# Optimization experiments

Measured on AMD Instinct MI355X. Metric: run time of the kernel, lower is better.

## Reference

```python
import jax, jax.numpy as jnp
import numpy as np
from math import sqrt

B, Q, S, D, H = 2, 2048, 2048, 1024, 16
ADIM = D // H
IEPS = 1e-32


def setup_inputs() -> dict:
    key = jax.random.key(0)
    ks = jax.random.split(key, 7)
    sc = 0.02
    return {
        "iQ": jax.random.normal(ks[0], (B, Q, D), jnp.float32),
        "iK": jax.random.normal(ks[1], (B, S, D), jnp.float32),
        "mask": jax.random.randint(ks[2], (B, Q, S), 0, 2) > 0,
        "Wq": jax.random.normal(ks[3], (D, D), jnp.float32) * sc,
        "Wkv": jax.random.normal(ks[4], (2 * D, D), jnp.float32) * sc,
        "Wo": jax.random.normal(ks[5], (D, D), jnp.float32) * sc,
        "nbias": jnp.zeros((1,), jnp.float32),
    }


def sparse_norm(scores, nbias):
    # ReLU(x + b)^2 normalized along last axis (SparseNormer)
    t = jax.nn.relu(scores + nbias[0])
    t = t * t
    return t / (t.sum(-1, keepdims=True) + IEPS)


def reference(iQ, iK, mask, Wq, Wkv, Wo, nbias):
    b, q, _ = iQ.shape
    s = iK.shape[1]
    # projections (no bias)
    rq = (iQ @ Wq.T).reshape(b, q, H, ADIM)            # bqhd
    kv = (iK @ Wkv.T).reshape(b, s, 2, H, ADIM)
    rk, rv = kv[:, :, 0], kv[:, :, 1]                  # bshd each
    scores = jnp.einsum("bqhd,bshd->bhqs", rq, rk) / sqrt(ADIM)
    scores = jnp.where(mask[:, None, :, :], jnp.float32(-1e32), scores)
    attn = sparse_norm(scores, nbias)
    o = jnp.einsum("bhqs,bshd->bqhd", attn, rv).reshape(b, q, H * ADIM)
    return o @ Wo.T
```

## Files before the change

### kernel.cpp

```cpp
#include <hip/hip_runtime.h>

#define Bb 2
#define Qq 2048
#define Ss 2048
#define Dd 1024
#define Hh 16
#define AD 64
#define KK 1024

typedef __attribute__((ext_vector_type(8))) short bf16x8;
typedef __attribute__((ext_vector_type(4))) short bf16x4;
typedef __attribute__((ext_vector_type(4))) float f32x4;
typedef unsigned short u16;
typedef unsigned int u32;
typedef unsigned long long u64;

__device__ __forceinline__ u16 f2bf(float f) {
  union { float f; u32 u; } v; v.f = f;
  u32 r = v.u + 0x7fffu + ((v.u >> 16) & 1u);
  return (u16)(r >> 16);
}

__device__ __forceinline__ void gld16(const u16* g, u16* l) {
  __builtin_amdgcn_global_load_lds(
      (const __attribute__((address_space(1))) unsigned int*)g,
      (__attribute__((address_space(3))) unsigned int*)l, 16, 0, 0);
}

__global__ __launch_bounds__(256) void cast_all_k(const float* __restrict__ iQ,
                                                  const float* __restrict__ iK,
                                                  const float* __restrict__ Wq,
                                                  const float* __restrict__ Wkv,
                                                  const float* __restrict__ Wo,
                                                  u16* __restrict__ Qb, u16* __restrict__ Kb,
                                                  u16* __restrict__ Wqb, u16* __restrict__ Wkvb,
                                                  u16* __restrict__ Wob) {
  int i = blockIdx.x * 256 + threadIdx.x;
  const float* src; u16* dst; int off;
  if (i < 1048576)      { src = iQ;  dst = Qb;   off = 0; }
  else if (i < 2097152) { src = iK;  dst = Kb;   off = 1048576; }
  else if (i < 2359296) { src = Wq;  dst = Wqb;  off = 2097152; }
  else if (i < 2883584) { src = Wkv; dst = Wkvb; off = 2359296; }
  else                  { src = Wo;  dst = Wob;  off = 2883584; }
  int j = i - off;
  float4 v = ((const float4*)src)[j];
  ushort4 o;
  o.x = f2bf(v.x); o.y = f2bf(v.y); o.z = f2bf(v.z); o.w = f2bf(v.w);
  ((ushort4*)dst)[j] = o;
}

__global__ __launch_bounds__(256) void maskpack_k(const int* __restrict__ mask,
                                                  u64* __restrict__ mb64) {
  int flat = blockIdx.x * 256 + threadIdx.x;
  int st = flat & 31;
  int q  = (flat >> 5) & 2047;
  int b  = flat >> 16;
  const int4* src = (const int4*)(mask + ((size_t)(b * Qq + q)) * Ss + st * 64);
  u64 bits = 0;
#pragma unroll
  for (int c = 0; c < 16; c++) {
    int4 v = src[c];
    bits |= (u64)(v.x != 0) << (c * 4 + 0);
    bits |= (u64)(v.y != 0) << (c * 4 + 1);
    bits |= (u64)(v.z != 0) << (c * 4 + 2);
    bits |= (u64)(v.w != 0) << (c * 4 + 3);
  }
  mb64[flat] = bits;
}

__global__ __launch_bounds__(256, 4) void proj_k(const u16* __restrict__ Qb,
                                                 const u16* __restrict__ Kb,
                                                 const u16* __restrict__ Wqb,
                                                 const u16* __restrict__ Wkvb,
                                                 u16* __restrict__ RQ,
                                                 u16* __restrict__ KV,
                                                 u16* __restrict__ VT) {
  __shared__ u16 LDS[128 * 64 + 64 * 64];
  u16* As = LDS;
  u16* Ws = LDS + 128 * 64;
  u16* Tt = LDS;
  const int tid = threadIdx.x;
  const int lane = tid & 63, wave = tid >> 6;
  const int qr = lane & 15, quad = lane >> 4;
  const int bid = blockIdx.x;
  const bool isQ = bid < 512;
  const int b2 = isQ ? bid : bid - 512;
  const int m0 = (b2 & 31) * 128;
  const int n0 = (b2 >> 5) * 64;
  const u16* A = isQ ? Qb : Kb;
  const u16* W = isQ ? Wqb : Wkvb;
  const int wm = (wave >> 1) * 64, wn = (wave & 1) * 32;
  const int qs = qr & 7;

  const int sr = tid >> 3, sc = tid & 7;
  const u16 *aP[4], *wP[2];
  u16 *aL[4], *wL[2];
#pragma unroll
  for (int is = 0; is < 4; is++) {
    int row = is * 32 + sr;
    aP[is] = A + (size_t)(m0 + row) * KK + ((sc ^ (row & 7)) * 8);
    aL[is] = As + row * 64 + sc * 8;
  }
#pragma unroll
  for (int is = 0; is < 2; is++) {
    int row = is * 32 + sr;
    wP[is] = W + (size_t)(n0 + row) * KK + ((sc ^ (row & 7)) * 8);
    wL[is] = Ws + row * 64 + sc * 8;
  }

  f32x4 acc[4][2] = {};

  for (int k0 = 0; k0 < KK; k0 += 64) {
#pragma unroll
    for (int is = 0; is < 4; is++) gld16(aP[is] + k0, aL[is]);
#pragma unroll
    for (int is = 0; is < 2; is++) gld16(wP[is] + k0, wL[is]);
    __syncthreads();
#pragma unroll
    for (int kk = 0; kk < 2; kk++) {
      bf16x8 af[4], bw[2];
#pragma unroll
      for (int i = 0; i < 4; i++)
        af[i] = *(const bf16x8*)(As + (wm + i * 16 + qr) * 64 + (((kk * 4 + quad) ^ qs) * 8));
#pragma unroll
      for (int j = 0; j < 2; j++)
        bw[j] = *(const bf16x8*)(Ws + (wn + j * 16 + qr) * 64 + (((kk * 4 + quad) ^ qs) * 8));
#pragma unroll
      for (int i = 0; i < 4; i++)
#pragma unroll
        for (int j = 0; j < 2; j++)
          acc[i][j] = __builtin_amdgcn_mfma_f32_16x16x32_bf16(af[i], bw[j], acc[i][j], 0, 0, 0);
    }
    __syncthreads();
  }

  if (isQ) {
#pragma unroll
    for (int i = 0; i < 4; i++)
#pragma unroll
      for (int j = 0; j < 2; j++)
#pragma unroll
        for (int r = 0; r < 4; r++) {
          int row = m0 + wm + i * 16 + quad * 4 + r;
          int col = n0 + wn + j * 16 + qr;
          RQ[(size_t)row * 1024 + col] = f2bf(acc[i][j][r] * 0.125f);
        }
  } else if (n0 < 1024) {
#pragma unroll
    for (int i = 0; i < 4; i++)
#pragma unroll
      for (int j = 0; j < 2; j++)
#pragma unroll
        for (int r = 0; r < 4; r++) {
          int row = m0 + wm + i * 16 + quad * 4 + r;
          int col = n0 + wn + j * 16 + qr;
          KV[(size_t)row * 2048 + col] = f2bf(acc[i][j][r]);
        }
  } else {
#pragma unroll
    for (int i = 0; i < 4; i++)
#pragma unroll
      for (int j = 0; j < 2; j++)
#pragma unroll
        for (int r = 0; r < 4; r++) {
          int srow = wm + i * 16 + quad * 4 + r;
          int d    = wn + j * 16 + qr;
          Tt[d * 136 + srow] = f2bf(acc[i][j][r]);
        }
    __syncthreads();
    const int h = (n0 - 1024) >> 6;
    const int bb = m0 >> 11, sbase = m0 & 2047;
    u16* vdst = VT + (((size_t)(bb * Hh + h)) * AD) * Ss;
    const int d = tid >> 2;
#pragma unroll
    for (int ic = 0; ic < 4; ic++) {
      int ch = ic * 4 + (tid & 3);
      *(int4*)(vdst + (size_t)d * Ss + sbase + ch * 8) = *(const int4*)(Tt + d * 136 + ch * 8);
    }
  }
}

__global__ __launch_bounds__(256, 4) void oproj_k(const u16* __restrict__ A,
                                                  const u16* __restrict__ W,
                                                  float* __restrict__ C) {
  __shared__ u16 LDS[128 * 64 + 64 * 64];
  u16* As = LDS;
  u16* Ws = LDS + 128 * 64;
  const int tid = threadIdx.x;
  const int lane = tid & 63, wave = tid >> 6;
  const int qr = lane & 15, quad = lane >> 4;
  const int m0 = (blockIdx.x & 31) * 128;
  const int n0 = (blockIdx.x >> 5) * 64;
  const int wm = (wave >> 1) * 64, wn = (wave & 1) * 32;
  const int qs = qr & 7;
  const int sr = tid >> 3, sc = tid & 7;
  const u16 *aP[4], *wP[2];
  u16 *aL[4], *wL[2];
#pragma unroll
  for (int is = 0; is < 4; is++) {
    int row = is * 32 + sr;
    aP[is] = A + (size_t)(m0 + row) * KK + ((sc ^ (row & 7)) * 8);
    aL[is] = As + row * 64 + sc * 8;
  }
#pragma unroll
  for (int is = 0; is < 2; is++) {
    int row = is * 32 + sr;
    wP[is] = W + (size_t)(n0 + row) * KK + ((sc ^ (row & 7)) * 8);
    wL[is] = Ws + row * 64 + sc * 8;
  }
  f32x4 acc[4][2] = {};
  for (int k0 = 0; k0 < KK; k0 += 64) {
#pragma unroll
    for (int is = 0; is < 4; is++) gld16(aP[is] + k0, aL[is]);
#pragma unroll
    for (int is = 0; is < 2; is++) gld16(wP[is] + k0, wL[is]);
    __syncthreads();
#pragma unroll
    for (int kk = 0; kk < 2; kk++) {
      bf16x8 af[4], bw[2];
#pragma unroll
      for (int i = 0; i < 4; i++)
        af[i] = *(const bf16x8*)(As + (wm + i * 16 + qr) * 64 + (((kk * 4 + quad) ^ qs) * 8));
#pragma unroll
      for (int j = 0; j < 2; j++)
        bw[j] = *(const bf16x8*)(Ws + (wn + j * 16 + qr) * 64 + (((kk * 4 + quad) ^ qs) * 8));
#pragma unroll
      for (int i = 0; i < 4; i++)
#pragma unroll
        for (int j = 0; j < 2; j++)
          acc[i][j] = __builtin_amdgcn_mfma_f32_16x16x32_bf16(af[i], bw[j], acc[i][j], 0, 0, 0);
    }
    __syncthreads();
  }
#pragma unroll
  for (int i = 0; i < 4; i++)
#pragma unroll
    for (int j = 0; j < 2; j++)
#pragma unroll
      for (int r = 0; r < 4; r++) {
        int row = m0 + wm + i * 16 + quad * 4 + r;
        int col = n0 + wn + j * 16 + qr;
        C[(size_t)row * 1024 + col] = acc[i][j][r];
      }
}

__global__ __launch_bounds__(512, 4) void attn_k(const u16* __restrict__ RQ,
                                                 const u16* __restrict__ KV,
                                                 const u16* __restrict__ VT,
                                                 const u64* __restrict__ mb64,
                                                 const float* __restrict__ nbias,
                                                 u16* __restrict__ O) {
  __shared__ char LB[65536];
  u16* Ks  = (u16*)LB;
  u16* Vts = (u16*)(LB + 32768);
  f32x4* Xch = (f32x4*)LB;

  const int tid = threadIdx.x, lane = tid & 63, w = tid >> 6;
  const int qh = w >> 1, sh = w & 1;
  const int qr = lane & 15, quad = lane >> 4;
  const int quad4 = quad * 4, qs = qr & 7;
  const int q0 = blockIdx.x * 128, h = blockIdx.y, b = blockIdx.z;
  const u16* rqb = RQ + ((size_t)(b * Qq + q0)) * Dd + h * AD;
  const u16* kb  = KV + ((size_t)b * Ss) * 2048 + h * AD;
  const u16* vtb = VT + ((size_t)(b * Hh + h)) * AD * Ss;
  const u64* mbase = mb64 + ((size_t)(b * Qq + q0)) * 32;
  const float nb = nbias[0];

  bf16x8 bq[2][2];
#pragma unroll
  for (int j = 0; j < 2; j++)
#pragma unroll
    for (int kk = 0; kk < 2; kk++)
      bq[j][kk] = *(const bf16x8*)(rqb + (size_t)(qh * 32 + j * 16 + qr) * Dd +
                                   kk * 32 + quad * 8);

  const u16 *kP[4], *vP[4];
  u16 *kL[4], *vL[4];
  {
    const int r8 = tid >> 3, c8 = tid & 7;
#pragma unroll
    for (int is = 0; is < 4; is++) {
      int row = is * 64 + r8;
      kP[is] = kb + (size_t)row * 2048 + ((c8 ^ (row & 7)) * 8);
      kL[is] = Ks + row * 64 + c8 * 8;
    }
    const int r32 = tid >> 5, c32 = tid & 31;
#pragma unroll
    for (int is = 0; is < 4; is++) {
      int row = is * 16 + r32;
      vP[is] = vtb + (size_t)row * Ss + ((c32 ^ (row & 7)) * 8);
      vL[is] = Vts + row * 256 + c32 * 8;
    }
  }

  const bf16x4 vones = { (short)0x3F80, (short)0x3F80, (short)0x3F80, (short)0x3F80 };
  f32x4 acc[2][4] = {};
  f32x4 accd[2] = {};

  const u16* kfr = Ks + (sh * 128 + qr) * 64;
  const u16* kfr0 = kfr + ((quad ^ qs) * 8);
  const u16* kfr1 = kfr + (((quad + 4) ^ qs) * 8);

  for (int t = 0; t < 8; t++) {
    __syncthreads();
#pragma unroll
    for (int is = 0; is < 4; is++) gld16(kP[is] + (size_t)t * 524288, kL[is]);
#pragma unroll
    for (int is = 0; is < 4; is++) gld16(vP[is] + t * 256, vL[is]);
    u64 mw[2][2];
#pragma unroll
    for (int j = 0; j < 2; j++) {
      const u64* mp = mbase + (size_t)(qh * 32 + j * 16 + qr) * 32 + t * 4 + sh * 2;
      mw[j][0] = mp[0];
      mw[j][1] = mp[1];
    }
    __syncthreads();

#pragma unroll
    for (int mi = 0; mi < 8; mi++) {
      bf16x8 ak0 = *(const bf16x8*)(kfr0 + mi * 1024);
      bf16x8 ak1 = *(const bf16x8*)(kfr1 + mi * 1024);
      f32x4 asc0 = { nb, nb, nb, nb };
      f32x4 asc1 = { nb, nb, nb, nb };
      asc0 = __builtin_amdgcn_mfma_f32_16x16x32_bf16(ak0, bq[0][0], asc0, 0, 0, 0);
      asc0 = __builtin_amdgcn_mfma_f32_16x16x32_bf16(ak1, bq[0][1], asc0, 0, 0, 0);
      asc1 = __builtin_amdgcn_mfma_f32_16x16x32_bf16(ak0, bq[1][0], asc1, 0, 0, 0);
      asc1 = __builtin_amdgcn_mfma_f32_16x16x32_bf16(ak1, bq[1][1], asc1, 0, 0, 0);

      union { u32 w2[2]; bf16x4 v; } pk[2];
#pragma unroll
      for (int j = 0; j < 2; j++) {
        f32x4 asc = j ? asc1 : asc0;
        u32 mm = (u32)(mw[j][mi >> 2] >> ((mi & 3) * 16 + quad4)) & 0xFu;
        u32 th[4];
#pragma unroll
        for (int r = 0; r < 4; r++) {
          float tt = fmaxf(asc[r], 0.f);
          tt = tt * tt;
          if ((mm >> r) & 1) tt = 0.f;
          union { float f; u32 u; } cv; cv.f = tt;
          th[r] = cv.u;
        }
        pk[j].w2[0] = __builtin_amdgcn_perm(th[1], th[0], 0x07060302u);
        pk[j].w2[1] = __builtin_amdgcn_perm(th[3], th[2], 0x07060302u);
        accd[j] = __builtin_amdgcn_mfma_f32_16x16x16bf16_1k(pk[j].v, vones, accd[j], 0, 0, 0);
      }
      int g = ((sh * 32 + mi * 4 + quad) ^ (qs << 1)) * 4;
#pragma unroll
      for (int nn = 0; nn < 4; nn++) {
        bf16x4 bv = *(const bf16x4*)(Vts + (nn * 16 + qr) * 256 + g);
        acc[0][nn] = __builtin_amdgcn_mfma_f32_16x16x16bf16_1k(pk[0].v, bv, acc[0][nn], 0, 0, 0);
        acc[1][nn] = __builtin_amdgcn_mfma_f32_16x16x16bf16_1k(pk[1].v, bv, acc[1][nn], 0, 0, 0);
      }
    }
  }

  __syncthreads();
  if (sh == 1) {
#pragma unroll
    for (int j = 0; j < 2; j++) {
#pragma unroll
      for (int nn = 0; nn < 4; nn++)
        Xch[qh * 640 + (j * 4 + nn) * 64 + lane] = acc[j][nn];
      Xch[qh * 640 + (8 + j) * 64 + lane] = accd[j];
    }
  }
  __syncthreads();
  if (sh == 0) {
    u16* ob = O + ((size_t)(b * Qq + q0)) * Dd + h * AD;
#pragma unroll
    for (int j = 0; j < 2; j++) {
      f32x4 dpart = Xch[qh * 640 + (8 + j) * 64 + lane];
      float rc[4];
#pragma unroll
      for (int r = 0; r < 4; r++)
        rc[r] = 1.f / (accd[j][r] + dpart[r] + 1e-32f);
#pragma unroll
      for (int nn = 0; nn < 4; nn++) {
        f32x4 p4 = Xch[qh * 640 + (j * 4 + nn) * 64 + lane];
#pragma unroll
        for (int r = 0; r < 4; r++) {
          int ql = qh * 32 + j * 16 + quad * 4 + r;
          ob[(size_t)ql * Dd + nn * 16 + qr] = f2bf((acc[j][nn][r] + p4[r]) * rc[r]);
        }
      }
    }
  }
}

extern "C" void kernel_launch(void* const* d_in, const int* in_sizes, int n_in,
                              void* d_out, int out_size, void* d_ws, size_t ws_size,
                              hipStream_t stream) {
  const float* iQ   = (const float*)d_in[0];
  const float* iK   = (const float*)d_in[1];
  const int*   mask = (const int*)d_in[2];
  const float* Wq   = (const float*)d_in[3];
  const float* Wkv  = (const float*)d_in[4];
  const float* Wo   = (const float*)d_in[5];
  const float* nb   = (const float*)d_in[6];

  char* ws = (char*)d_ws;
  u16* Qb   = (u16*)(ws + (size_t)0);
  u16* Kb   = (u16*)(ws + ((size_t)8  << 20));
  u16* Wqb  = (u16*)(ws + ((size_t)16 << 20));
  u16* Wkvb = (u16*)(ws + ((size_t)18 << 20));
  u16* Wob  = (u16*)(ws + ((size_t)22 << 20));
  u16* RQ   = (u16*)(ws + ((size_t)24 << 20));
  u16* KV   = (u16*)(ws + ((size_t)32 << 20));
  u16* Obuf = (u16*)(ws + ((size_t)48 << 20));
  u16* VT   = (u16*)(ws + ((size_t)56 << 20));
  u64* MB   = (u64*)(ws + ((size_t)64 << 20));

  cast_all_k<<<12288, 256, 0, stream>>>(iQ, iK, Wq, Wkv, Wo, Qb, Kb, Wqb, Wkvb, Wob);
  maskpack_k<<<512, 256, 0, stream>>>(mask, MB);

  proj_k<<<1536, 256, 0, stream>>>(Qb, Kb, Wqb, Wkvb, RQ, KV, VT);

  attn_k<<<dim3(16, 16, 2), 512, 0, stream>>>(RQ, KV, VT, MB, nb, Obuf);

  oproj_k<<<512, 256, 0, stream>>>(Obuf, Wob, (float*)d_out);
}
```

Before: 229.3 us.

## Enlarge GEMM tiles to 128x128, compact K buffer, merge mask pack into cast

Projection and output GEMMs move from 128x64 to 128x128 block tiles, so each wave computes 64x64 and the number of blocks halves. This raises MFMA work per LDS load and cuts redundant global reads of the A operand, at the cost of more accumulator registers, which is why the occupancy hint drops from 4 to 3. The K projection is now written to a compact 1024-wide buffer instead of a 2048-stride KV buffer, so attention reads K with a tighter stride. The mask-packing kernel is folded into the cast kernel to save one launch.

```diff
diff --git a/kernel.cpp b/kernel.cpp
--- a/kernel.cpp
+++ b/kernel.cpp
@@ -32,103 +32,101 @@
                                                   const float* __restrict__ Wq,
                                                   const float* __restrict__ Wkv,
                                                   const float* __restrict__ Wo,
+                                                  const int* __restrict__ mask,
                                                   u16* __restrict__ Qb, u16* __restrict__ Kb,
                                                   u16* __restrict__ Wqb, u16* __restrict__ Wkvb,
-                                                  u16* __restrict__ Wob) {
+                                                  u16* __restrict__ Wob,
+                                                  u64* __restrict__ mb64) {
   int i = blockIdx.x * 256 + threadIdx.x;
-  const float* src; u16* dst; int off;
-  if (i < 1048576)      { src = iQ;  dst = Qb;   off = 0; }
-  else if (i < 2097152) { src = iK;  dst = Kb;   off = 1048576; }
-  else if (i < 2359296) { src = Wq;  dst = Wqb;  off = 2097152; }
-  else if (i < 2883584) { src = Wkv; dst = Wkvb; off = 2359296; }
-  else                  { src = Wo;  dst = Wob;  off = 2883584; }
-  int j = i - off;
-  float4 v = ((const float4*)src)[j];
-  ushort4 o;
-  o.x = f2bf(v.x); o.y = f2bf(v.y); o.z = f2bf(v.z); o.w = f2bf(v.w);
-  ((ushort4*)dst)[j] = o;
-}
-
-__global__ __launch_bounds__(256) void maskpack_k(const int* __restrict__ mask,
-                                                  u64* __restrict__ mb64) {
-  int flat = blockIdx.x * 256 + threadIdx.x;
-  int st = flat & 31;
-  int q  = (flat >> 5) & 2047;
-  int b  = flat >> 16;
-  const int4* src = (const int4*)(mask + ((size_t)(b * Qq + q)) * Ss + st * 64);
-  u64 bits = 0;
-#pragma unroll
-  for (int c = 0; c < 16; c++) {
-    int4 v = src[c];
-    bits |= (u64)(v.x != 0) << (c * 4 + 0);
-    bits |= (u64)(v.y != 0) << (c * 4 + 1);
-    bits |= (u64)(v.z != 0) << (c * 4 + 2);
-    bits |= (u64)(v.w != 0) << (c * 4 + 3);
-  }
-  mb64[flat] = bits;
-}
-
-__global__ __launch_bounds__(256, 4) void proj_k(const u16* __restrict__ Qb,
+  if (i < 3145728) {
+    const float* src; u16* dst; int off;
+    if (i < 1048576)      { src = iQ;  dst = Qb;   off = 0; }
+    else if (i < 2097152) { src = iK;  dst = Kb;   off = 1048576; }
+    else if (i < 2359296) { src = Wq;  dst = Wqb;  off = 2097152; }
+    else if (i < 2883584) { src = Wkv; dst = Wkvb; off = 2359296; }
+    else                  { src = Wo;  dst = Wob;  off = 2883584; }
+    int j = i - off;
+    float4 v = ((const float4*)src)[j];
+    ushort4 o;
+    o.x = f2bf(v.x); o.y = f2bf(v.y); o.z = f2bf(v.z); o.w = f2bf(v.w);
+    ((ushort4*)dst)[j] = o;
+  } else {
+    int flat = i - 3145728;
+    int st = flat & 31;
+    int q  = (flat >> 5) & 2047;
+    int b  = flat >> 16;
+    const int4* src = (const int4*)(mask + ((size_t)(b * Qq + q)) * Ss + st * 64);
+    u64 bits = 0;
+#pragma unroll
+    for (int c = 0; c < 16; c++) {
+      int4 v = src[c];
+      bits |= (u64)(v.x != 0) << (c * 4 + 0);
+      bits |= (u64)(v.y != 0) << (c * 4 + 1);
+      bits |= (u64)(v.z != 0) << (c * 4 + 2);
+      bits |= (u64)(v.w != 0) << (c * 4 + 3);
+    }
+    mb64[flat] = bits;
+  }
+}
+
+__global__ __launch_bounds__(256, 3) void proj_k(const u16* __restrict__ Qb,
                                                  const u16* __restrict__ Kb,
                                                  const u16* __restrict__ Wqb,
                                                  const u16* __restrict__ Wkvb,
                                                  u16* __restrict__ RQ,
-                                                 u16* __restrict__ KV,
+                                                 u16* __restrict__ Kc,
                                                  u16* __restrict__ VT) {
-  __shared__ u16 LDS[128 * 64 + 64 * 64];
-  u16* As = LDS;
-  u16* Ws = LDS + 128 * 64;
-  u16* Tt = LDS;
+  __shared__ char LB[34816];
+  u16* As = (u16*)LB;
+  u16* Ws = (u16*)(LB + 16384);
   const int tid = threadIdx.x;
   const int lane = tid & 63, wave = tid >> 6;
   const int qr = lane & 15, quad = lane >> 4;
+  const int qs = qr & 7;
   const int bid = blockIdx.x;
-  const bool isQ = bid < 512;
-  const int b2 = isQ ? bid : bid - 512;
+  const bool isQ = bid < 256;
+  const int b2 = isQ ? bid : bid - 256;
   const int m0 = (b2 & 31) * 128;
-  const int n0 = (b2 >> 5) * 64;
+  const int n0 = (b2 >> 5) * 128;
   const u16* A = isQ ? Qb : Kb;
   const u16* W = isQ ? Wqb : Wkvb;
-  const int wm = (wave >> 1) * 64, wn = (wave & 1) * 32;
-  const int qs = qr & 7;
+  const int wm = (wave >> 1) * 64, wn = (wave & 1) * 64;
 
   const int sr = tid >> 3, sc = tid & 7;
-  const u16 *aP[4], *wP[2];
-  u16 *aL[4], *wL[2];
+  const u16 *aP[4], *wP[4];
+  u16 *aL[4], *wL[4];
 #pragma unroll
   for (int is = 0; is < 4; is++) {
     int row = is * 32 + sr;
-    aP[is] = A + (size_t)(m0 + row) * KK + ((sc ^ (row & 7)) * 8);
+    int goff = (sc ^ (row & 7)) * 8;
+    aP[is] = A + (size_t)(m0 + row) * KK + goff;
+    wP[is] = W + (size_t)(n0 + row) * KK + goff;
     aL[is] = As + row * 64 + sc * 8;
-  }
-#pragma unroll
-  for (int is = 0; is < 2; is++) {
-    int row = is * 32 + sr;
-    wP[is] = W + (size_t)(n0 + row) * KK + ((sc ^ (row & 7)) * 8);
     wL[is] = Ws + row * 64 + sc * 8;
   }
 
-  f32x4 acc[4][2] = {};
+  f32x4 acc[4][4] = {};
 
   for (int k0 = 0; k0 < KK; k0 += 64) {
 #pragma unroll
     for (int is = 0; is < 4; is++) gld16(aP[is] + k0, aL[is]);
 #pragma unroll
-    for (int is = 0; is < 2; is++) gld16(wP[is] + k0, wL[is]);
+    for (int is = 0; is < 4; is++) gld16(wP[is] + k0, wL[is]);
     __syncthreads();
 #pragma unroll
     for (int kk = 0; kk < 2; kk++) {
-      bf16x8 af[4], bw[2];
+      bf16x8 af[4], bw[4];
+      int ch = ((kk * 4 + quad) ^ qs) * 8;
 #pragma unroll
       for (int i = 0; i < 4; i++)
-        af[i] = *(const bf16x8*)(As + (wm + i * 16 + qr) * 64 + (((kk * 4 + quad) ^ qs) * 8));
-#pragma unroll
-      for (int j = 0; j < 2; j++)
-        bw[j] = *(const bf16x8*)(Ws + (wn + j * 16 + qr) * 64 + (((kk * 4 + quad) ^ qs) * 8));
+        af[i] = *(const bf16x8*)(As + (wm + i * 16 + qr) * 64 + ch);
+#pragma unroll
+      for (int j = 0; j < 4; j++)
+        bw[j] = *(const bf16x8*)(Ws + (wn + j * 16 + qr) * 64 + ch);
 #pragma unroll
       for (int i = 0; i < 4; i++)
 #pragma unroll
-        for (int j = 0; j < 2; j++)
+        for (int j = 0; j < 4; j++)
           acc[i][j] = __builtin_amdgcn_mfma_f32_16x16x32_bf16(af[i], bw[j], acc[i][j], 0, 0, 0);
     }
     __syncthreads();
@@ -138,7 +136,7 @@
 #pragma unroll
     for (int i = 0; i < 4; i++)
 #pragma unroll
-      for (int j = 0; j < 2; j++)
+      for (int j = 0; j < 4; j++)
 #pragma unroll
         for (int r = 0; r < 4; r++) {
           int row = m0 + wm + i * 16 + quad * 4 + r;
@@ -149,85 +147,84 @@
 #pragma unroll
     for (int i = 0; i < 4; i++)
 #pragma unroll
-      for (int j = 0; j < 2; j++)
+      for (int j = 0; j < 4; j++)
 #pragma unroll
         for (int r = 0; r < 4; r++) {
           int row = m0 + wm + i * 16 + quad * 4 + r;
           int col = n0 + wn + j * 16 + qr;
-          KV[(size_t)row * 2048 + col] = f2bf(acc[i][j][r]);
+          Kc[(size_t)row * 1024 + col] = f2bf(acc[i][j][r]);
         }
   } else {
+    u16* Ttp = (u16*)LB + (wn >> 6) * (64 * 136);
 #pragma unroll
     for (int i = 0; i < 4; i++)
 #pragma unroll
-      for (int j = 0; j < 2; j++)
+      for (int j = 0; j < 4; j++)
 #pragma unroll
         for (int r = 0; r < 4; r++) {
           int srow = wm + i * 16 + quad * 4 + r;
-          int d    = wn + j * 16 + qr;
-          Tt[d * 136 + srow] = f2bf(acc[i][j][r]);
+          int d    = j * 16 + qr;
+          Ttp[d * 136 + srow] = f2bf(acc[i][j][r]);
         }
     __syncthreads();
-    const int h = (n0 - 1024) >> 6;
+    const int h0 = (n0 - 1024) >> 6;
     const int bb = m0 >> 11, sbase = m0 & 2047;
-    u16* vdst = VT + (((size_t)(bb * Hh + h)) * AD) * Ss;
-    const int d = tid >> 2;
-#pragma unroll
-    for (int ic = 0; ic < 4; ic++) {
-      int ch = ic * 4 + (tid & 3);
-      *(int4*)(vdst + (size_t)d * Ss + sbase + ch * 8) = *(const int4*)(Tt + d * 136 + ch * 8);
-    }
-  }
-}
-
-__global__ __launch_bounds__(256, 4) void oproj_k(const u16* __restrict__ A,
+    const u16* LB16 = (const u16*)LB;
+#pragma unroll
+    for (int ic = 0; ic < 8; ic++) {
+      int flat = ic * 256 + tid;
+      int hd = flat >> 10, d = (flat >> 4) & 63, ch = flat & 15;
+      *(int4*)(VT + (((size_t)(bb * Hh + h0 + hd)) * AD + d) * Ss + sbase + ch * 8) =
+          *(const int4*)(LB16 + hd * (64 * 136) + d * 136 + ch * 8);
+    }
+  }
+}
+
+__global__ __launch_bounds__(256, 3) void oproj_k(const u16* __restrict__ A,
                                                   const u16* __restrict__ W,
                                                   float* __restrict__ C) {
-  __shared__ u16 LDS[128 * 64 + 64 * 64];
-  u16* As = LDS;
-  u16* Ws = LDS + 128 * 64;
+  __shared__ u16 As[128 * 64];
+  __shared__ u16 Ws[128 * 64];
   const int tid = threadIdx.x;
   const int lane = tid & 63, wave = tid >> 6;
   const int qr = lane & 15, quad = lane >> 4;
+  const int qs = qr & 7;
   const int m0 = (blockIdx.x & 31) * 128;
-  const int n0 = (blockIdx.x >> 5) * 64;
-  const int wm = (wave >> 1) * 64, wn = (wave & 1) * 32;
-  const int qs = qr & 7;
+  const int n0 = (blockIdx.x >> 5) * 128;
+  const int wm = (wave >> 1) * 64, wn = (wave & 1) * 64;
   const int sr = tid >> 3, sc = tid & 7;
-  const u16 *aP[4], *wP[2];
-  u16 *aL[4], *wL[2];
+  const u16 *aP[4], *wP[4];
+  u16 *aL[4], *wL[4];
 #pragma unroll
   for (int is = 0; is < 4; is++) {
     int row = is * 32 + sr;
-    aP[is] = A + (size_t)(m0 + row) * KK + ((sc ^ (row & 7)) * 8);
+    int goff = (sc ^ (row & 7)) * 8;
+    aP[is] = A + (size_t)(m0 + row) * KK + goff;
+    wP[is] = W + (size_t)(n0 + row) * KK + goff;
     aL[is] = As + row * 64 + sc * 8;
-  }
-#pragma unroll
-  for (int is = 0; is < 2; is++) {
-    int row = is * 32 + sr;
-    wP[is] = W + (size_t)(n0 + row) * KK + ((sc ^ (row & 7)) * 8);
     wL[is] = Ws + row * 64 + sc * 8;
   }
-  f32x4 acc[4][2] = {};
+  f32x4 acc[4][4] = {};
   for (int k0 = 0; k0 < KK; k0 += 64) {
 #pragma unroll
     for (int is = 0; is < 4; is++) gld16(aP[is] + k0, aL[is]);
 #pragma unroll
-    for (int is = 0; is < 2; is++) gld16(wP[is] + k0, wL[is]);
+    for (int is = 0; is < 4; is++) gld16(wP[is] + k0, wL[is]);
     __syncthreads();
 #pragma unroll
     for (int kk = 0; kk < 2; kk++) {
-      bf16x8 af[4], bw[2];
+      bf16x8 af[4], bw[4];
+      int ch = ((kk * 4 + quad) ^ qs) * 8;
 #pragma unroll
       for (int i = 0; i < 4; i++)
-        af[i] = *(const bf16x8*)(As + (wm + i * 16 + qr) * 64 + (((kk * 4 + quad) ^ qs) * 8));
-#pragma unroll
-      for (int j = 0; j < 2; j++)
-        bw[j] = *(const bf16x8*)(Ws + (wn + j * 16 + qr) * 64 + (((kk * 4 + quad) ^ qs) * 8));
+        af[i] = *(const bf16x8*)(As + (wm + i * 16 + qr) * 64 + ch);
+#pragma unroll
+      for (int j = 0; j < 4; j++)
+        bw[j] = *(const bf16x8*)(Ws + (wn + j * 16 + qr) * 64 + ch);
 #pragma unroll
       for (int i = 0; i < 4; i++)
 #pragma unroll
-        for (int j = 0; j < 2; j++)
+        for (int j = 0; j < 4; j++)
           acc[i][j] = __builtin_amdgcn_mfma_f32_16x16x32_bf16(af[i], bw[j], acc[i][j], 0, 0, 0);
     }
     __syncthreads();
@@ -235,7 +232,7 @@
 #pragma unroll
   for (int i = 0; i < 4; i++)
 #pragma unroll
-    for (int j = 0; j < 2; j++)
+    for (int j = 0; j < 4; j++)
 #pragma unroll
       for (int r = 0; r < 4; r++) {
         int row = m0 + wm + i * 16 + quad * 4 + r;
@@ -245,7 +242,7 @@
 }
 
 __global__ __launch_bounds__(512, 4) void attn_k(const u16* __restrict__ RQ,
-                                                 const u16* __restrict__ KV,
+                                                 const u16* __restrict__ Kc,
                                                  const u16* __restrict__ VT,
                                                  const u64* __restrict__ mb64,
                                                  const float* __restrict__ nbias,
@@ -261,7 +258,7 @@
   const int quad4 = quad * 4, qs = qr & 7;
   const int q0 = blockIdx.x * 128, h = blockIdx.y, b = blockIdx.z;
   const u16* rqb = RQ + ((size_t)(b * Qq + q0)) * Dd + h * AD;
-  const u16* kb  = KV + ((size_t)b * Ss) * 2048 + h * AD;
+  const u16* kb  = Kc + ((size_t)b * Ss) * 1024 + h * AD;
   const u16* vtb = VT + ((size_t)(b * Hh + h)) * AD * Ss;
   const u64* mbase = mb64 + ((size_t)(b * Qq + q0)) * 32;
   const float nb = nbias[0];
@@ -281,7 +278,7 @@
 #pragma unroll
     for (int is = 0; is < 4; is++) {
       int row = is * 64 + r8;
-      kP[is] = kb + (size_t)row * 2048 + ((c8 ^ (row & 7)) * 8);
+      kP[is] = kb + (size_t)row * 1024 + ((c8 ^ (row & 7)) * 8);
       kL[is] = Ks + row * 64 + c8 * 8;
     }
     const int r32 = tid >> 5, c32 = tid & 31;
@@ -304,7 +301,7 @@
   for (int t = 0; t < 8; t++) {
     __syncthreads();
 #pragma unroll
-    for (int is = 0; is < 4; is++) gld16(kP[is] + (size_t)t * 524288, kL[is]);
+    for (int is = 0; is < 4; is++) gld16(kP[is] + (size_t)t * 262144, kL[is]);
 #pragma unroll
     for (int is = 0; is < 4; is++) gld16(vP[is] + t * 256, vL[is]);
     u64 mw[2][2];
@@ -406,17 +403,17 @@
   u16* Wkvb = (u16*)(ws + ((size_t)18 << 20));
   u16* Wob  = (u16*)(ws + ((size_t)22 << 20));
   u16* RQ   = (u16*)(ws + ((size_t)24 << 20));
-  u16* KV   = (u16*)(ws + ((size_t)32 << 20));
+  u16* Kc   = (u16*)(ws + ((size_t)32 << 20));
   u16* Obuf = (u16*)(ws + ((size_t)48 << 20));
   u16* VT   = (u16*)(ws + ((size_t)56 << 20));
   u64* MB   = (u64*)(ws + ((size_t)64 << 20));
 
-  cast_all_k<<<12288, 256, 0, stream>>>(iQ, iK, Wq, Wkv, Wo, Qb, Kb, Wqb, Wkvb, Wob);
-  maskpack_k<<<512, 256, 0, stream>>>(mask, MB);
-
-  proj_k<<<1536, 256, 0, stream>>>(Qb, Kb, Wqb, Wkvb, RQ, KV, VT);
-
-  attn_k<<<dim3(16, 16, 2), 512, 0, stream>>>(RQ, KV, VT, MB, nb, Obuf);
-
-  oproj_k<<<512, 256, 0, stream>>>(Obuf, Wob, (float*)d_out);
-}
+  cast_all_k<<<12800, 256, 0, stream>>>(iQ, iK, Wq, Wkv, Wo, mask,
+                                        Qb, Kb, Wqb, Wkvb, Wob, MB);
+
+  proj_k<<<768, 256, 0, stream>>>(Qb, Kb, Wqb, Wkvb, RQ, Kc, VT);
+
+  attn_k<<<dim3(16, 16, 2), 512, 0, stream>>>(RQ, Kc, VT, MB, nb, Obuf);
+
+  oproj_k<<<256, 256, 0, stream>>>(Obuf, Wob, (float*)d_out);
+}
```

Result: slower. 244.5 us (+6.6%).
